# Optimization experiments

Measured on AMD Instinct MI355X. Metric: run time of the kernel, lower is better.

The kernel has to match this reference:

```python
import jax, jax.numpy as jnp
import numpy as np

EPS = 1e-18
MARGIN = 0.2  # hp.margin (cancels: positive/positive == 1)
BIAS = 1.0    # hp.bias


def setup_inputs() -> dict:
    key = jax.random.key(0)
    k1, k2, k3, k4 = jax.random.split(key, 4)
    B, T, D = 32, 256, 256  # T == D required by the broadcast in Ecos_sim
    return {
        "pre_VF": jax.random.normal(k1, (B, T, D), dtype=jnp.float32),
        "pre_AF": jax.random.normal(k2, (B, T, D), dtype=jnp.float32),
        "back_VF": jax.random.normal(k3, (B, T, D), dtype=jnp.float32),
        "back_AF": jax.random.normal(k4, (B, T, D), dtype=jnp.float32),
    }


def _direction_loss(V, A):
    """For each anchor i: log(1 + sum_{j != i} exp(sim(V_i, A_j))).

    sim(V_i, A_j)[t, s] = (V_i @ A_j.T)[t, s] / (||V_i||_F * colnorm(A_j)[s])
    (faithful to Ecos_sim: scalar Frobenius norm for V, per-column norm for A,
    broadcast along the last axis; positive/positive == 1 exactly, so the
    positive term and margin cancel.)
    """
    B = V.shape[0]
    # upper[i,j,t,s] = <V[i,t,:], A[j,s,:]>
    upper = jnp.einsum("itd,jsd->ijts", V, A)
    v_norm = jnp.sqrt(jnp.sum(V ** 2, axis=(1, 2)) + EPS)      # [B]
    a_norm = jnp.sqrt(jnp.sum(A ** 2, axis=1) + EPS)           # [B, D]
    sim = upper / (v_norm[:, None, None, None] * a_norm[None, :, None, :])
    e_sim = jnp.exp(sim)                                        # [B,B,T,T]
    idx = jnp.arange(B)
    down = e_sim.sum(axis=1) - e_sim[idx, idx]                  # exclude j == i
    rows = jnp.log(1.0 + down)                                  # [B,T,T]
    return rows.reshape(-1, rows.shape[-1])                     # cat along dim 0


def reference(pre_VF, pre_AF, back_VF, back_AF):
    sim_back_V = _direction_loss(back_VF, back_AF)
    sim_back_A = _direction_loss(back_AF, back_VF)
    return -(1.0 / BIAS) * (sim_back_V + sim_back_A)
```

## Files before the change

### kernel.cpp

```cpp
#include <hip/hip_runtime.h>
#include <cstdint>

#define R_TOT 8192
#define KD    256
#define SLOT  ((size_t)R_TOT * KD)
#define IVN_OFF  0
#define ICN_OFF  256
#define CSQ_OFF  (ICN_OFF + 65536)
#define MATS_OFF (CSQ_OFF + 524288)

typedef float f32x4 __attribute__((ext_vector_type(4)));
typedef int   i32x4 __attribute__((ext_vector_type(4)));
typedef int   i32x8 __attribute__((ext_vector_type(8)));

__device__ __forceinline__ void glds16(const void* g, void* l){
  __builtin_amdgcn_global_load_lds((const __attribute__((address_space(1))) uint32_t*)g,
                                   (__attribute__((address_space(3))) uint32_t*)l, 16, 0, 0);
}

__global__ void cast_ns_k(const float* __restrict__ V, const float* __restrict__ A,
                          unsigned char* __restrict__ mats, float* __restrict__ csq){
  const int tc = blockIdx.x, j = blockIdx.y, ten = blockIdx.z;
  const int tid = threadIdx.x;
  const int g    = tid & 31;
  const int tsub = tid >> 5;
  const int c    = g >> 1;
  const int half = g & 1;
  const float* X = (ten ? A : V) + (size_t)j * 65536;
  unsigned char* M = mats + (size_t)ten * SLOT + (size_t)j * 65536;
  float cs[8];
  #pragma unroll
  for (int e = 0; e < 8; ++e) cs[e] = 0.f;
  #pragma unroll
  for (int tt = 0; tt < 4; ++tt){
    const int t = tc * 32 + tt * 8 + tsub;
    const float4 p0 = *(const float4*)(X + t * 256 + g * 8);
    const float4 p1 = *(const float4*)(X + t * 256 + g * 8 + 4);
    cs[0] += p0.x * p0.x; cs[1] += p0.y * p0.y; cs[2] += p0.z * p0.z; cs[3] += p0.w * p0.w;
    cs[4] += p1.x * p1.x; cs[5] += p1.y * p1.y; cs[6] += p1.z * p1.z; cs[7] += p1.w * p1.w;
    int d0 = __builtin_amdgcn_cvt_pk_fp8_f32(p0.x, p0.y, 0, false);
    d0     = __builtin_amdgcn_cvt_pk_fp8_f32(p0.z, p0.w, d0, true);
    int d1 = __builtin_amdgcn_cvt_pk_fp8_f32(p1.x, p1.y, 0, false);
    d1     = __builtin_amdgcn_cvt_pk_fp8_f32(p1.z, p1.w, d1, true);
    int2 o; o.x = d0; o.y = d1;
    *(int2*)(M + (size_t)t * 256 + (((c ^ (t & 15)) << 4) | (half << 3))) = o;
  }
  __shared__ float red[8][256];
  #pragma unroll
  for (int e = 0; e < 8; ++e) red[tsub][g * 8 + e] = cs[e];
  __syncthreads();
  float s = 0.f;
  #pragma unroll
  for (int gg = 0; gg < 8; ++gg) s += red[gg][tid];
  csq[(size_t)((tc * 2 + ten) * 32 + j) * 256 + tid] = s;
}

__global__ void nreduce_k(const float* __restrict__ csq, float* __restrict__ ivn,
                          float* __restrict__ icn){
  const int j = blockIdx.x, ten = blockIdx.y, s = threadIdx.x;
  float c = 0.f;
  #pragma unroll
  for (int tc = 0; tc < 8; ++tc)
    c += csq[(size_t)((tc * 2 + ten) * 32 + j) * 256 + s];
  icn[ten * 8192 + j * 256 + s] = rsqrtf(c + 1e-18f);
  __shared__ float red[256];
  red[s] = c; __syncthreads();
  for (int off = 128; off > 0; off >>= 1){
    if (s < off) red[s] += red[s + off];
    __syncthreads();
  }
  if (s == 0) ivn[ten * 32 + j] = rsqrtf(red[0] + 1e-18f);
}

__global__ __launch_bounds__(256, 2) void gemm_both_k(const unsigned char* __restrict__ mats,
                                                      const float* __restrict__ ivn,
                                                      const float* __restrict__ icn,
                                                      float* __restrict__ out){
  __shared__ __align__(16) char smem[40960];
  const int tid  = threadIdx.x;
  const int lane = tid & 63;
  const int w    = tid >> 6;
  const int dir  = w >> 1;
  const int wn   = (w & 1) * 16;
  const int lm   = lane & 15;
  const int kh   = lane >> 4;
  const int s0   = blockIdx.x * 32;
  const int rb   = blockIdx.y;
  const int r0   = rb * 64;
  const int ib   = rb >> 2;

  const unsigned char* rowmat = mats + (size_t)dir * SLOT;
  const unsigned char* colmat = mats + (size_t)(1 - dir) * SLOT;
  const float sivn = ivn[dir * 32 + ib] * 1.44269504088896340736f;

  char* wbase = smem + w * 8192;
  float* cscw = (float*)(smem + 32768) + w * 512;
  const int lo16 = lane * 16;
  const unsigned char* colbase = colmat + (size_t)(s0 + wn) * 256;

  auto issue = [&](int x){
    const int j = x + (x >= ib ? 1 : 0);
    const unsigned char* src = colbase + (size_t)j * 65536;
    char* dst = wbase + ((x & 1) << 12);
    #pragma unroll
    for (int c = 0; c < 4; ++c)
      glds16(src + c * 1024 + lo16, dst + c * 1024 + lo16);
  };

  issue(0);

  {
    const float* ibase = icn + (size_t)(1 - dir) * 8192 + s0 + wn;
    #pragma unroll
    for (int jx = 0; jx < 8; ++jx){
      const int j = kh * 8 + jx;
      cscw[j * 16 + lm] = sivn * ibase[j * 256 + lm];
    }
  }

  i32x8 afr[4][2];
  #pragma unroll
  for (int mi = 0; mi < 4; ++mi){
    const unsigned char* rp = rowmat + (size_t)(r0 + mi * 16 + lm) * 256;
    #pragma unroll
    for (int t = 0; t < 2; ++t){
      i32x4 lo = *(const i32x4*)(rp + ((((t << 3) | (kh << 1) | 0) ^ lm) << 4));
      i32x4 hi = *(const i32x4*)(rp + ((((t << 3) | (kh << 1) | 1) ^ lm) << 4));
      afr[mi][t] = i32x8{lo.x, lo.y, lo.z, lo.w, hi.x, hi.y, hi.z, hi.w};
    }
  }
  #pragma unroll
  for (int mi = 0; mi < 4; ++mi)
    #pragma unroll
    for (int t = 0; t < 2; ++t)
      asm volatile("" : "+v"(afr[mi][t]));

  int ad[2][2];
  #pragma unroll
  for (int t = 0; t < 2; ++t)
    #pragma unroll
    for (int u = 0; u < 2; ++u)
      ad[t][u] = lm * 256 + ((((t << 3) | (kh << 1) | u) ^ lm) << 4);

  f32x4 acc[4];
  #pragma unroll
  for (int mi = 0; mi < 4; ++mi)
    acc[mi] = f32x4{0.f, 0.f, 0.f, 0.f};
  const f32x4 fz = {0.f, 0.f, 0.f, 0.f};

  i32x8 bA[2], bB[2];
  f32x4 SA[4], SB[4];
  float cscA, cscB;

#define DSREAD(BX, CX, x_) do{                                                  \
    const char* rbuf_ = wbase + (((x_) & 1) << 12);                             \
    i32x4 lo0_ = *(const i32x4*)(rbuf_ + ad[0][0]);                             \
    i32x4 hi0_ = *(const i32x4*)(rbuf_ + ad[0][1]);                             \
    i32x4 lo1_ = *(const i32x4*)(rbuf_ + ad[1][0]);                             \
    i32x4 hi1_ = *(const i32x4*)(rbuf_ + ad[1][1]);                             \
    BX[0] = i32x8{lo0_.x, lo0_.y, lo0_.z, lo0_.w, hi0_.x, hi0_.y, hi0_.z, hi0_.w}; \
    BX[1] = i32x8{lo1_.x, lo1_.y, lo1_.z, lo1_.w, hi1_.x, hi1_.y, hi1_.z, hi1_.w}; \
    const int j_ = (x_) + ((x_) >= ib ? 1 : 0);                                 \
    CX = cscw[j_ * 16 + lm];                                                    \
  }while(0)

#define MFMA8(SX, BX) do{                                                       \
    SX[0] = __builtin_amdgcn_mfma_scale_f32_16x16x128_f8f6f4(afr[0][0], BX[0], fz,    0, 0, 0, 127, 0, 127); \
    SX[1] = __builtin_amdgcn_mfma_scale_f32_16x16x128_f8f6f4(afr[1][0], BX[0], fz,    0, 0, 0, 127, 0, 127); \
    SX[2] = __builtin_amdgcn_mfma_scale_f32_16x16x128_f8f6f4(afr[2][0], BX[0], fz,    0, 0, 0, 127, 0, 127); \
    SX[3] = __builtin_amdgcn_mfma_scale_f32_16x16x128_f8f6f4(afr[3][0], BX[0], fz,    0, 0, 0, 127, 0, 127); \
    SX[0] = __builtin_amdgcn_mfma_scale_f32_16x16x128_f8f6f4(afr[0][1], BX[1], SX[0], 0, 0, 0, 127, 0, 127); \
    SX[1] = __builtin_amdgcn_mfma_scale_f32_16x16x128_f8f6f4(afr[1][1], BX[1], SX[1], 0, 0, 0, 127, 0, 127); \
    SX[2] = __builtin_amdgcn_mfma_scale_f32_16x16x128_f8f6f4(afr[2][1], BX[1], SX[2], 0, 0, 0, 127, 0, 127); \
    SX[3] = __builtin_amdgcn_mfma_scale_f32_16x16x128_f8f6f4(afr[3][1], BX[1], SX[3], 0, 0, 0, 127, 0, 127); \
  }while(0)

#define EXPACC(SY, CY) do{                                                      \
    _Pragma("unroll")                                                           \
    for (int mi_ = 0; mi_ < 4; ++mi_){                                          \
      _Pragma("unroll")                                                         \
      for (int r_ = 0; r_ < 4; ++r_)                                            \
        acc[mi_][r_] += __builtin_amdgcn_exp2f(SY[mi_][r_] * CY);               \
    }                                                                           \
  }while(0)

#define STEP(x_, BX, SX, CX, SY, CY, PF) do{                                    \
    if (PF) issue((x_) + 1);                                                    \
    if (PF) asm volatile("s_waitcnt vmcnt(4)" ::: "memory");                    \
    else    asm volatile("s_waitcnt vmcnt(0)" ::: "memory");                    \
    DSREAD(BX, CX, x_);                                                         \
    asm volatile("s_waitcnt lgkmcnt(0)" ::: "memory");                          \
    __builtin_amdgcn_sched_barrier(0);                                          \
    __builtin_amdgcn_s_setprio(1);                                              \
    MFMA8(SX, BX);                                                              \
    EXPACC(SY, CY);                                                             \
    __builtin_amdgcn_s_setprio(0);                                              \
  }while(0)

  asm volatile("s_waitcnt vmcnt(0) lgkmcnt(0)" ::: "memory");
  __builtin_amdgcn_sched_barrier(0);
  DSREAD(bA, cscA, 0);
  issue(1);
  asm volatile("s_waitcnt lgkmcnt(0)" ::: "memory");
  __builtin_amdgcn_sched_barrier(0);
  __builtin_amdgcn_s_setprio(1);
  MFMA8(SA, bA);
  __builtin_amdgcn_s_setprio(0);

  #pragma unroll 1
  for (int it = 0; it < 14; ++it){
    STEP(2 * it + 1, bB, SB, cscB, SA, cscA, 1);
    STEP(2 * it + 2, bA, SA, cscA, SB, cscB, 1);
  }
  STEP(29, bB, SB, cscB, SA, cscA, 1);
  STEP(30, bA, SA, cscA, SB, cscB, 0);
  EXPACC(SA, cscA);

#undef STEP
#undef EXPACC
#undef MFMA8
#undef DSREAD

  __syncthreads();
  float* ebuf = (float*)smem;
  #pragma unroll
  for (int mi = 0; mi < 4; ++mi){
    const int n = wn + lm;
    #pragma unroll
    for (int r = 0; r < 4; ++r){
      const int m = mi * 16 + (kh << 2) + r;
      ebuf[(dir * 64 + m) * 36 + n] = __logf(1.f + acc[mi][r]);
    }
  }
  __syncthreads();
  #pragma unroll
  for (int p = 0; p < 2; ++p){
    const int i   = tid + p * 256;
    const int row = i >> 3;
    const int c4  = i & 7;
    const f32x4 e0 = *(const f32x4*)(&ebuf[row * 36 + c4 * 4]);
    const f32x4 e1 = *(const f32x4*)(&ebuf[(64 + row) * 36 + c4 * 4]);
    f32x4 o;
    #pragma unroll
    for (int e = 0; e < 4; ++e) o[e] = -(e0[e] + e1[e]);
    *(f32x4*)(&out[(size_t)(r0 + row) * 256 + s0 + c4 * 4]) = o;
  }
}

extern "C" void kernel_launch(void* const* d_in, const int* in_sizes, int n_in,
                              void* d_out, int out_size, void* d_ws, size_t ws_size,
                              hipStream_t stream){
  const float* V = (const float*)d_in[2];
  const float* A = (const float*)d_in[3];
  float* out = (float*)d_out;
  float* ivn = (float*)((char*)d_ws + IVN_OFF);
  float* icn = (float*)((char*)d_ws + ICN_OFF);
  float* csq = (float*)((char*)d_ws + CSQ_OFF);
  unsigned char* mats = (unsigned char*)((char*)d_ws + MATS_OFF);

  cast_ns_k<<<dim3(8, 32, 2), 256, 0, stream>>>(V, A, mats, csq);
  nreduce_k<<<dim3(32, 2), 256, 0, stream>>>(csq, ivn, icn);
  gemm_both_k<<<dim3(8, 128), 256, 0, stream>>>(mats, ivn, icn, out);
}
```

Before: 118.1 us.

## Deepen MFMA pipeline with two-ahead prefetch and raise occupancy bound

Restructures the fused GEMM-exp main loop. Global-to-LDS loads are now issued two tiles ahead, and the next tile's B fragment is read from LDS before the current tile's MFMAs run, so LDS latency overlaps the matrix work. The per-column scale load is split out and done after the exp accumulation. The launch bound goes from 2 to 3 blocks per CU, which caps registers per thread and may cause spills given the large register-resident A fragments and score buffers.

```diff
diff --git a/kernel.cpp b/kernel.cpp
--- a/kernel.cpp
+++ b/kernel.cpp
@@ -72,7 +72,7 @@
   if (s == 0) ivn[ten * 32 + j] = rsqrtf(red[0] + 1e-18f);
 }
 
-__global__ __launch_bounds__(256, 2) void gemm_both_k(const unsigned char* __restrict__ mats,
+__global__ __launch_bounds__(256, 3) void gemm_both_k(const unsigned char* __restrict__ mats,
                                                       const float* __restrict__ ivn,
                                                       const float* __restrict__ icn,
                                                       float* __restrict__ out){
@@ -135,6 +135,8 @@
     for (int t = 0; t < 2; ++t)
       asm volatile("" : "+v"(afr[mi][t]));
 
+  issue(1);
+
   int ad[2][2];
   #pragma unroll
   for (int t = 0; t < 2; ++t)
@@ -152,14 +154,17 @@
   f32x4 SA[4], SB[4];
   float cscA, cscB;
 
-#define DSREAD(BX, CX, x_) do{                                                  \
-    const char* rbuf_ = wbase + (((x_) & 1) << 12);                             \
+#define DSREADB(BX, xp_) do{                                                    \
+    const char* rbuf_ = wbase + (((xp_) & 1) << 12);                            \
     i32x4 lo0_ = *(const i32x4*)(rbuf_ + ad[0][0]);                             \
     i32x4 hi0_ = *(const i32x4*)(rbuf_ + ad[0][1]);                             \
     i32x4 lo1_ = *(const i32x4*)(rbuf_ + ad[1][0]);                             \
     i32x4 hi1_ = *(const i32x4*)(rbuf_ + ad[1][1]);                             \
     BX[0] = i32x8{lo0_.x, lo0_.y, lo0_.z, lo0_.w, hi0_.x, hi0_.y, hi0_.z, hi0_.w}; \
     BX[1] = i32x8{lo1_.x, lo1_.y, lo1_.z, lo1_.w, hi1_.x, hi1_.y, hi1_.z, hi1_.w}; \
+  }while(0)
+
+#define CSCLD(CX, x_) do{                                                       \
     const int j_ = (x_) + ((x_) >= ib ? 1 : 0);                                 \
     CX = cscw[j_ * 16 + lm];                                                    \
   }while(0)
@@ -184,42 +189,66 @@
     }                                                                           \
   }while(0)
 
-#define STEP(x_, BX, SX, CX, SY, CY, PF) do{                                    \
-    if (PF) issue((x_) + 1);                                                    \
-    if (PF) asm volatile("s_waitcnt vmcnt(4)" ::: "memory");                    \
-    else    asm volatile("s_waitcnt vmcnt(0)" ::: "memory");                    \
-    DSREAD(BX, CX, x_);                                                         \
+#define STEP_FULL(x_, BC, BN, SC, SP, CP) do{                                   \
+    issue((x_) + 2);                                                            \
+    asm volatile("s_waitcnt vmcnt(4)" ::: "memory");                            \
+    DSREADB(BN, (x_) + 1);                                                      \
+    __builtin_amdgcn_sched_barrier(0);                                          \
+    __builtin_amdgcn_s_setprio(1);                                              \
+    MFMA8(SC, BC);                                                              \
+    __builtin_amdgcn_s_setprio(0);                                              \
+    EXPACC(SP, CP);                                                             \
+    CSCLD(CP, (x_) + 1);                                                        \
     asm volatile("s_waitcnt lgkmcnt(0)" ::: "memory");                          \
     __builtin_amdgcn_sched_barrier(0);                                          \
-    __builtin_amdgcn_s_setprio(1);                                              \
-    MFMA8(SX, BX);                                                              \
-    EXPACC(SY, CY);                                                             \
-    __builtin_amdgcn_s_setprio(0);                                              \
-  }while(0)
-
-  asm volatile("s_waitcnt vmcnt(0) lgkmcnt(0)" ::: "memory");
-  __builtin_amdgcn_sched_barrier(0);
-  DSREAD(bA, cscA, 0);
-  issue(1);
+  }while(0)
+
+  asm volatile("s_waitcnt vmcnt(4) lgkmcnt(0)" ::: "memory");
+  __builtin_amdgcn_sched_barrier(0);
+  DSREADB(bA, 0);
+  CSCLD(cscA, 0);
   asm volatile("s_waitcnt lgkmcnt(0)" ::: "memory");
+  __builtin_amdgcn_sched_barrier(0);
+
+  issue(2);
+  asm volatile("s_waitcnt vmcnt(4)" ::: "memory");
+  DSREADB(bB, 1);
   __builtin_amdgcn_sched_barrier(0);
   __builtin_amdgcn_s_setprio(1);
   MFMA8(SA, bA);
   __builtin_amdgcn_s_setprio(0);
+  CSCLD(cscB, 1);
+  asm volatile("s_waitcnt lgkmcnt(0)" ::: "memory");
+  __builtin_amdgcn_sched_barrier(0);
 
   #pragma unroll 1
   for (int it = 0; it < 14; ++it){
-    STEP(2 * it + 1, bB, SB, cscB, SA, cscA, 1);
-    STEP(2 * it + 2, bA, SA, cscA, SB, cscB, 1);
-  }
-  STEP(29, bB, SB, cscB, SA, cscA, 1);
-  STEP(30, bA, SA, cscA, SB, cscB, 0);
+    STEP_FULL(2 * it + 1, bB, bA, SB, SA, cscA);
+    STEP_FULL(2 * it + 2, bA, bB, SA, SB, cscB);
+  }
+
+  asm volatile("s_waitcnt vmcnt(0)" ::: "memory");
+  DSREADB(bA, 30);
+  __builtin_amdgcn_sched_barrier(0);
+  __builtin_amdgcn_s_setprio(1);
+  MFMA8(SB, bB);
+  __builtin_amdgcn_s_setprio(0);
   EXPACC(SA, cscA);
-
-#undef STEP
+  CSCLD(cscA, 30);
+  asm volatile("s_waitcnt lgkmcnt(0)" ::: "memory");
+  __builtin_amdgcn_sched_barrier(0);
+
+  __builtin_amdgcn_s_setprio(1);
+  MFMA8(SA, bA);
+  __builtin_amdgcn_s_setprio(0);
+  EXPACC(SB, cscB);
+  EXPACC(SA, cscA);
+
+#undef STEP_FULL
 #undef EXPACC
 #undef MFMA8
-#undef DSREAD
+#undef CSCLD
+#undef DSREADB
 
   __syncthreads();
   float* ebuf = (float*)smem;
```

Result: slower. 254.1 us (+115.0%).

## Load B fragments directly from global into registers, dropping LDS staging

Applied to the files above, without the earlier changes.

Replaces the global_load_lds double-buffered staging of column fp8 tiles with direct per-lane global vector loads into registers, software-pipelined one step ahead. This shrinks shared memory from 40 KB to 26 KB and raises the launch-bounds occupancy hint from 2 to 3 blocks per CU. It also drops the explicit waitcnt, setprio and sched_barrier control and the S register double buffer, leaving scheduling to the compiler. The tradeoff is that global load latency is now exposed directly in the MFMA loop and there is no explicit vmcnt or priority control.

```diff
diff --git a/kernel.cpp b/kernel.cpp
--- a/kernel.cpp
+++ b/kernel.cpp
@@ -12,11 +12,6 @@
 typedef float f32x4 __attribute__((ext_vector_type(4)));
 typedef int   i32x4 __attribute__((ext_vector_type(4)));
 typedef int   i32x8 __attribute__((ext_vector_type(8)));
-
-__device__ __forceinline__ void glds16(const void* g, void* l){
-  __builtin_amdgcn_global_load_lds((const __attribute__((address_space(1))) uint32_t*)g,
-                                   (__attribute__((address_space(3))) uint32_t*)l, 16, 0, 0);
-}
 
 __global__ void cast_ns_k(const float* __restrict__ V, const float* __restrict__ A,
                           unsigned char* __restrict__ mats, float* __restrict__ csq){
@@ -72,11 +67,11 @@
   if (s == 0) ivn[ten * 32 + j] = rsqrtf(red[0] + 1e-18f);
 }
 
-__global__ __launch_bounds__(256, 2) void gemm_both_k(const unsigned char* __restrict__ mats,
+__global__ __launch_bounds__(256, 3) void gemm_both_k(const unsigned char* __restrict__ mats,
                                                       const float* __restrict__ ivn,
                                                       const float* __restrict__ icn,
                                                       float* __restrict__ out){
-  __shared__ __align__(16) char smem[40960];
+  __shared__ __align__(16) char smem[26624];
   const int tid  = threadIdx.x;
   const int lane = tid & 63;
   const int w    = tid >> 6;
@@ -93,21 +88,9 @@
   const unsigned char* colmat = mats + (size_t)(1 - dir) * SLOT;
   const float sivn = ivn[dir * 32 + ib] * 1.44269504088896340736f;
 
-  char* wbase = smem + w * 8192;
-  float* cscw = (float*)(smem + 32768) + w * 512;
-  const int lo16 = lane * 16;
+  float* ebuf = (float*)smem;
+  float* cscw = (float*)(smem + 18432) + w * 512;
   const unsigned char* colbase = colmat + (size_t)(s0 + wn) * 256;
-
-  auto issue = [&](int x){
-    const int j = x + (x >= ib ? 1 : 0);
-    const unsigned char* src = colbase + (size_t)j * 65536;
-    char* dst = wbase + ((x & 1) << 12);
-    #pragma unroll
-    for (int c = 0; c < 4; ++c)
-      glds16(src + c * 1024 + lo16, dst + c * 1024 + lo16);
-  };
-
-  issue(0);
 
   {
     const float* ibase = icn + (size_t)(1 - dir) * 8192 + s0 + wn;
@@ -135,12 +118,12 @@
     for (int t = 0; t < 2; ++t)
       asm volatile("" : "+v"(afr[mi][t]));
 
-  int ad[2][2];
+  int boff[2][2];
   #pragma unroll
   for (int t = 0; t < 2; ++t)
     #pragma unroll
     for (int u = 0; u < 2; ++u)
-      ad[t][u] = lm * 256 + ((((t << 3) | (kh << 1) | u) ^ lm) << 4);
+      boff[t][u] = lm * 256 + ((((t << 3) | (kh << 1) | u) ^ lm) << 4);
 
   f32x4 acc[4];
   #pragma unroll
@@ -149,80 +132,72 @@
   const f32x4 fz = {0.f, 0.f, 0.f, 0.f};
 
   i32x8 bA[2], bB[2];
-  f32x4 SA[4], SB[4];
+  f32x4 S[4];
   float cscA, cscB;
 
-#define DSREAD(BX, CX, x_) do{                                                  \
-    const char* rbuf_ = wbase + (((x_) & 1) << 12);                             \
-    i32x4 lo0_ = *(const i32x4*)(rbuf_ + ad[0][0]);                             \
-    i32x4 hi0_ = *(const i32x4*)(rbuf_ + ad[0][1]);                             \
-    i32x4 lo1_ = *(const i32x4*)(rbuf_ + ad[1][0]);                             \
-    i32x4 hi1_ = *(const i32x4*)(rbuf_ + ad[1][1]);                             \
+#define JOF(x_) ((x_) + ((x_) >= ib ? 1 : 0))
+
+#define LOADB(BX, x_) do{                                                       \
+    const unsigned char* p_ = colbase + (size_t)JOF(x_) * 65536;                \
+    i32x4 lo0_ = *(const i32x4*)(p_ + boff[0][0]);                              \
+    i32x4 hi0_ = *(const i32x4*)(p_ + boff[0][1]);                              \
+    i32x4 lo1_ = *(const i32x4*)(p_ + boff[1][0]);                              \
+    i32x4 hi1_ = *(const i32x4*)(p_ + boff[1][1]);                              \
     BX[0] = i32x8{lo0_.x, lo0_.y, lo0_.z, lo0_.w, hi0_.x, hi0_.y, hi0_.z, hi0_.w}; \
     BX[1] = i32x8{lo1_.x, lo1_.y, lo1_.z, lo1_.w, hi1_.x, hi1_.y, hi1_.z, hi1_.w}; \
-    const int j_ = (x_) + ((x_) >= ib ? 1 : 0);                                 \
-    CX = cscw[j_ * 16 + lm];                                                    \
   }while(0)
 
-#define MFMA8(SX, BX) do{                                                       \
-    SX[0] = __builtin_amdgcn_mfma_scale_f32_16x16x128_f8f6f4(afr[0][0], BX[0], fz,    0, 0, 0, 127, 0, 127); \
-    SX[1] = __builtin_amdgcn_mfma_scale_f32_16x16x128_f8f6f4(afr[1][0], BX[0], fz,    0, 0, 0, 127, 0, 127); \
-    SX[2] = __builtin_amdgcn_mfma_scale_f32_16x16x128_f8f6f4(afr[2][0], BX[0], fz,    0, 0, 0, 127, 0, 127); \
-    SX[3] = __builtin_amdgcn_mfma_scale_f32_16x16x128_f8f6f4(afr[3][0], BX[0], fz,    0, 0, 0, 127, 0, 127); \
-    SX[0] = __builtin_amdgcn_mfma_scale_f32_16x16x128_f8f6f4(afr[0][1], BX[1], SX[0], 0, 0, 0, 127, 0, 127); \
-    SX[1] = __builtin_amdgcn_mfma_scale_f32_16x16x128_f8f6f4(afr[1][1], BX[1], SX[1], 0, 0, 0, 127, 0, 127); \
-    SX[2] = __builtin_amdgcn_mfma_scale_f32_16x16x128_f8f6f4(afr[2][1], BX[1], SX[2], 0, 0, 0, 127, 0, 127); \
-    SX[3] = __builtin_amdgcn_mfma_scale_f32_16x16x128_f8f6f4(afr[3][1], BX[1], SX[3], 0, 0, 0, 127, 0, 127); \
+#define MFMA8(BX) do{                                                           \
+    S[0] = __builtin_amdgcn_mfma_scale_f32_16x16x128_f8f6f4(afr[0][0], BX[0], fz,   0, 0, 0, 127, 0, 127); \
+    S[1] = __builtin_amdgcn_mfma_scale_f32_16x16x128_f8f6f4(afr[1][0], BX[0], fz,   0, 0, 0, 127, 0, 127); \
+    S[2] = __builtin_amdgcn_mfma_scale_f32_16x16x128_f8f6f4(afr[2][0], BX[0], fz,   0, 0, 0, 127, 0, 127); \
+    S[3] = __builtin_amdgcn_mfma_scale_f32_16x16x128_f8f6f4(afr[3][0], BX[0], fz,   0, 0, 0, 127, 0, 127); \
+    S[0] = __builtin_amdgcn_mfma_scale_f32_16x16x128_f8f6f4(afr[0][1], BX[1], S[0], 0, 0, 0, 127, 0, 127); \
+    S[1] = __builtin_amdgcn_mfma_scale_f32_16x16x128_f8f6f4(afr[1][1], BX[1], S[1], 0, 0, 0, 127, 0, 127); \
+    S[2] = __builtin_amdgcn_mfma_scale_f32_16x16x128_f8f6f4(afr[2][1], BX[1], S[2], 0, 0, 0, 127, 0, 127); \
+    S[3] = __builtin_amdgcn_mfma_scale_f32_16x16x128_f8f6f4(afr[3][1], BX[1], S[3], 0, 0, 0, 127, 0, 127); \
   }while(0)
 
-#define EXPACC(SY, CY) do{                                                      \
+#define EXPACC(CY) do{                                                          \
     _Pragma("unroll")                                                           \
     for (int mi_ = 0; mi_ < 4; ++mi_){                                          \
       _Pragma("unroll")                                                         \
       for (int r_ = 0; r_ < 4; ++r_)                                            \
-        acc[mi_][r_] += __builtin_amdgcn_exp2f(SY[mi_][r_] * CY);               \
+        acc[mi_][r_] += __builtin_amdgcn_exp2f(S[mi_][r_] * CY);                \
     }                                                                           \
   }while(0)
 
-#define STEP(x_, BX, SX, CX, SY, CY, PF) do{                                    \
-    if (PF) issue((x_) + 1);                                                    \
-    if (PF) asm volatile("s_waitcnt vmcnt(4)" ::: "memory");                    \
-    else    asm volatile("s_waitcnt vmcnt(0)" ::: "memory");                    \
-    DSREAD(BX, CX, x_);                                                         \
-    asm volatile("s_waitcnt lgkmcnt(0)" ::: "memory");                          \
-    __builtin_amdgcn_sched_barrier(0);                                          \
-    __builtin_amdgcn_s_setprio(1);                                              \
-    MFMA8(SX, BX);                                                              \
-    EXPACC(SY, CY);                                                             \
-    __builtin_amdgcn_s_setprio(0);                                              \
-  }while(0)
-
-  asm volatile("s_waitcnt vmcnt(0) lgkmcnt(0)" ::: "memory");
-  __builtin_amdgcn_sched_barrier(0);
-  DSREAD(bA, cscA, 0);
-  issue(1);
-  asm volatile("s_waitcnt lgkmcnt(0)" ::: "memory");
-  __builtin_amdgcn_sched_barrier(0);
-  __builtin_amdgcn_s_setprio(1);
-  MFMA8(SA, bA);
-  __builtin_amdgcn_s_setprio(0);
+  LOADB(bA, 0);
+  LOADB(bB, 1);
+  cscA = cscw[JOF(0) * 16 + lm];
 
   #pragma unroll 1
   for (int it = 0; it < 14; ++it){
-    STEP(2 * it + 1, bB, SB, cscB, SA, cscA, 1);
-    STEP(2 * it + 2, bA, SA, cscA, SB, cscB, 1);
-  }
-  STEP(29, bB, SB, cscB, SA, cscA, 1);
-  STEP(30, bA, SA, cscA, SB, cscB, 0);
-  EXPACC(SA, cscA);
-
-#undef STEP
+    const int x0 = 2 * it;
+    MFMA8(bA);
+    cscB = cscw[JOF(x0 + 1) * 16 + lm];
+    LOADB(bA, x0 + 2);
+    EXPACC(cscA);
+    MFMA8(bB);
+    cscA = cscw[JOF(x0 + 2) * 16 + lm];
+    LOADB(bB, x0 + 3);
+    EXPACC(cscB);
+  }
+  MFMA8(bA);
+  cscB = cscw[JOF(29) * 16 + lm];
+  LOADB(bA, 30);
+  EXPACC(cscA);
+  MFMA8(bB);
+  cscA = cscw[JOF(30) * 16 + lm];
+  EXPACC(cscB);
+  MFMA8(bA);
+  EXPACC(cscA);
+
 #undef EXPACC
 #undef MFMA8
-#undef DSREAD
-
-  __syncthreads();
-  float* ebuf = (float*)smem;
+#undef LOADB
+#undef JOF
+
   #pragma unroll
   for (int mi = 0; mi < 4; ++mi){
     const int n = wn + lm;
```

Result: slower. 131.9 us (+11.7%).
